# Kernel tuning notes

Hardware: AMD Instinct MI355X
Metric: run time of the kernel (lower is better)

The kernel has to match this reference:

```python
import jax, jax.numpy as jnp
import numpy as np

N = 50000
E = 800000
IN_DIM = 128
HID = 64
HEADS = 4
OUT = 64


def _bn(x, g, b, eps=1e-5):
    # BatchNorm1d with batch statistics (biased var), as in train-mode normalization
    mu = x.mean(0)
    var = ((x - mu) ** 2).mean(0)
    return (x - mu) * jax.lax.rsqrt(var + eps) * g + b


def _gat(x, W, a_src, a_dst, bias, src, dst, heads, dim, concat):
    # PyG GATConv: h = xW; e_ij = LeakyReLU(a_src.h_j + a_dst.h_i); softmax over incoming edges of i
    n = x.shape[0]
    h = (x @ W).reshape(n, heads, dim)            # [N,H,D]
    es = (h * a_src).sum(-1)                      # [N,H]
    ed = (h * a_dst).sum(-1)                      # [N,H]
    e = jax.nn.leaky_relu(es[src] + ed[dst], 0.2)  # [E,H]
    emax = jax.ops.segment_max(e, dst, num_segments=n)
    w = jnp.exp(e - emax[dst])
    denom = jax.ops.segment_sum(w, dst, num_segments=n)
    alpha = w / (denom[dst] + 1e-16)              # [E,H]
    out = jax.ops.segment_sum(h[src] * alpha[:, :, None], dst, num_segments=n)  # [N,H,D]
    out = out.reshape(n, heads * dim) if concat else out.mean(axis=1)
    return out + bias


def _gcn(x, W, bias, src, dst):
    # PyG GCNConv with self-loops (already appended): D^{-1/2} A D^{-1/2} x W
    n = x.shape[0]
    h = x @ W
    deg = jax.ops.segment_sum(jnp.ones(src.shape[0], h.dtype), dst, num_segments=n)
    dinv = jax.lax.rsqrt(jnp.maximum(deg, 1e-12))
    norm = dinv[src] * dinv[dst]                  # [E]
    return jax.ops.segment_sum(h[src] * norm[:, None], dst, num_segments=n) + bias


def setup_inputs() -> dict:
    key = jax.random.key(0)
    ks = jax.random.split(key, 16)
    s = 0.1
    inp = {
        "x": jax.random.normal(ks[0], (N, IN_DIM), jnp.float32),
        "edge_index": jax.random.randint(ks[1], (2, E), 0, N, jnp.int64 if jax.config.jax_enable_x64 else jnp.int32),
        "edge_attr": jax.random.normal(ks[2], (E,), jnp.float32),
        # GAT layer 1
        "W1": jax.random.normal(ks[3], (IN_DIM, HEADS * HID), jnp.float32) * s,
        "att_src1": jax.random.normal(ks[4], (HEADS, HID), jnp.float32) * s,
        "att_dst1": jax.random.normal(ks[5], (HEADS, HID), jnp.float32) * s,
        "b1": jnp.zeros((HEADS * HID,), jnp.float32),
        "g1": jnp.ones((HEADS * HID,), jnp.float32),
        "beta1": jnp.zeros((HEADS * HID,), jnp.float32),
        # GCN
        "Wg": jax.random.normal(ks[6], (HEADS * HID, HID), jnp.float32) * s,
        "bg": jnp.zeros((HID,), jnp.float32),
        "g2": jnp.ones((HID,), jnp.float32),
        "beta2": jnp.zeros((HID,), jnp.float32),
        # GAT layer 2 (heads=1, concat=False)
        "W2": jax.random.normal(ks[7], (HID, OUT), jnp.float32) * s,
        "att_src2": jax.random.normal(ks[8], (1, OUT), jnp.float32) * s,
        "att_dst2": jax.random.normal(ks[9], (1, OUT), jnp.float32) * s,
        "b2": jnp.zeros((OUT,), jnp.float32),
        "g3": jnp.ones((OUT,), jnp.float32),
        "beta3": jnp.zeros((OUT,), jnp.float32),
        # projector
        "Wp1": jax.random.normal(ks[10], (OUT, 128), jnp.float32) * s,
        "bp1": jnp.zeros((128,), jnp.float32),
        "Wp2": jax.random.normal(ks[11], (128, 64), jnp.float32) * s,
        "bp2": jnp.zeros((64,), jnp.float32),
    }
    return inp


def reference(x, edge_index, edge_attr, W1, att_src1, att_dst1, b1, g1, beta1,
              Wg, bg, g2, beta2, W2, att_src2, att_dst2, b2, g3, beta3,
              Wp1, bp1, Wp2, bp2):
    # edge_attr is ignored by GATConv when edge_dim is None (PyG behavior)
    loop = jnp.arange(N, dtype=edge_index.dtype)
    src = jnp.concatenate([edge_index[0], loop])  # self-loops appended
    dst = jnp.concatenate([edge_index[1], loop])
    h = _gat(x, W1, att_src1, att_dst1, b1, src, dst, HEADS, HID, True)
    h = jax.nn.elu(_bn(h, g1, beta1))
    h = _gcn(h, Wg, bg, src, dst)
    h = jax.nn.relu(_bn(h, g2, beta2))
    h = _gat(h, W2, att_src2, att_dst2, b2, src, dst, 1, OUT, False)
    h = jax.nn.elu(_bn(h, g3, beta3))
    return jax.nn.relu(h @ Wp1 + bp1) @ Wp2 + bp2
```

## Files before the change

kernel.cpp:

```cpp
#include <hip/hip_runtime.h>
#include <math.h>

#define NN 50000
#define EE 800000
#define E2 850000
#define SCB 196
#define GXL 391

__device__ __forceinline__ float bf2f(unsigned short u) {
  return __uint_as_float(((unsigned int)u) << 16);
}
__device__ __forceinline__ unsigned short f2bf(float f) {
  unsigned int x = __float_as_uint(f);
  unsigned int r = (x + 0x7fffu + ((x >> 16) & 1u)) >> 16;
  return (unsigned short)r;
}

__device__ __forceinline__ float leaky(float x) { return x > 0.f ? x : 0.2f * x; }

__device__ __forceinline__ int edge_src(const int* ei, int e) {
  return (e < EE) ? ei[e] : (e - EE);
}
__device__ __forceinline__ int edge_dst(const int* ei, int e) {
  return (e < EE) ? ei[EE + e] : (e - EE);
}

__global__ void k_deg(const int* __restrict__ ei, int* __restrict__ deg) {
  int e = blockIdx.x * blockDim.x + threadIdx.x;
  if (e < E2) atomicAdd(&deg[edge_dst(ei, e)], 1);
}

__global__ __launch_bounds__(256) void k_scan1(const int* __restrict__ deg,
                                               int* __restrict__ partial) {
  __shared__ int sd[256];
  int i = blockIdx.x * 256 + threadIdx.x;
  sd[threadIdx.x] = (i < NN) ? deg[i] : 0;
  __syncthreads();
  for (int off = 128; off > 0; off >>= 1) {
    if (threadIdx.x < off) sd[threadIdx.x] += sd[threadIdx.x + off];
    __syncthreads();
  }
  if (threadIdx.x == 0) partial[blockIdx.x] = sd[0];
}

__global__ __launch_bounds__(256) void k_scan3(const int* __restrict__ deg,
                                               const int* __restrict__ partial,
                                               int* __restrict__ rowptr,
                                               int* __restrict__ cnt,
                                               float* __restrict__ dinv) {
  __shared__ int sp[256];
  __shared__ int sd[256];
  int t = threadIdx.x;
  sp[t] = (t < SCB) ? partial[t] : 0;
  __syncthreads();
  for (int off = 1; off < 256; off <<= 1) {
    int v = (t >= off) ? sp[t - off] : 0;
    __syncthreads();
    sp[t] += v;
    __syncthreads();
  }
  int base = (blockIdx.x == 0) ? 0 : sp[blockIdx.x - 1];
  int i = blockIdx.x * 256 + t;
  int v = (i < NN) ? deg[i] : 0;
  sd[t] = v;
  __syncthreads();
  for (int off = 1; off < 256; off <<= 1) {
    int u = (t >= off) ? sd[t - off] : 0;
    __syncthreads();
    sd[t] += u;
    __syncthreads();
  }
  if (i < NN) {
    int excl = base + sd[t] - v;
    rowptr[i] = excl;
    cnt[i] = excl;
    dinv[i] = rsqrtf((float)v);
  }
  if (i == 0) rowptr[NN] = E2;
}

__global__ void k_fill(const int* __restrict__ ei, int* __restrict__ cnt,
                       int* __restrict__ csr) {
  int e = blockIdx.x * blockDim.x + threadIdx.x;
  if (e >= E2) return;
  int d = edge_dst(ei, e);
  int s = edge_src(ei, e);
  int pos = atomicAdd(&cnt[d], 1);
  csr[pos] = s;
}

__global__ __launch_bounds__(256) void k_gemm(
    const float* __restrict__ A, const unsigned short* __restrict__ Abf,
    const float* __restrict__ B, const float* __restrict__ biasOut,
    const float* __restrict__ bnst, const float* __restrict__ bng,
    const float* __restrict__ bnb, int inAct, int outAct,
    float* __restrict__ Cf, unsigned short* __restrict__ Cbf,
    const float* __restrict__ rowScale,
    const float* __restrict__ attSrc, const float* __restrict__ attDst,
    float* __restrict__ esOut, float* __restrict__ edOut, int attMode,
    int M, int K, int NC) {
  __shared__ float As[32][132];
  __shared__ float Bs[32][68];
  __shared__ float sSc[256], sSh[256];
  int t = threadIdx.x;
  int tx = t & 15, ty = t >> 4;
  if (bnst) {
    int c = t;
    if (c < K) {
      float sum = 0.f, sq = 0.f;
      for (int cp = 0; cp < 32; ++cp) {
        sum += bnst[cp * 2 * K + c];
        sq += bnst[cp * 2 * K + K + c];
      }
      const float invN = 1.0f / (float)NN;
      float mu = sum * invN;
      float var = sq * invN - mu * mu;
      float rs = rsqrtf(var + 1e-5f);
      float sc = rs * bng[c];
      sSc[c] = sc;
      sSh[c] = fmaf(-mu, sc, bnb[c]);
    }
    __syncthreads();
  }
  int rowBase = blockIdx.x * 128;
  int colBase = blockIdx.y * 64;
  float acc[8][4];
#pragma unroll
  for (int i = 0; i < 8; ++i)
#pragma unroll
    for (int j = 0; j < 4; ++j) acc[i][j] = 0.f;

  int kq = t & 7;
  int r0 = t >> 3;
  for (int kc = 0; kc < K; kc += 32) {
#pragma unroll
    for (int i2 = 0; i2 < 4; ++i2) {
      int row = r0 + 32 * i2;
      int gr = rowBase + row;
      float4 av = make_float4(0.f, 0.f, 0.f, 0.f);
      if (gr < M) {
        if (Abf) {
          ushort4 u4 = *(const ushort4*)&Abf[(size_t)gr * K + kc + kq * 4];
          av = make_float4(bf2f(u4.x), bf2f(u4.y), bf2f(u4.z), bf2f(u4.w));
        } else {
          av = *(const float4*)&A[(size_t)gr * K + kc + kq * 4];
        }
      }
      if (bnst) {
        int c = kc + kq * 4;
        av.x = fmaf(av.x, sSc[c + 0], sSh[c + 0]);
        av.y = fmaf(av.y, sSc[c + 1], sSh[c + 1]);
        av.z = fmaf(av.z, sSc[c + 2], sSh[c + 2]);
        av.w = fmaf(av.w, sSc[c + 3], sSh[c + 3]);
      }
      if (inAct == 1) {
        av.x = fmaxf(av.x, 0.f); av.y = fmaxf(av.y, 0.f);
        av.z = fmaxf(av.z, 0.f); av.w = fmaxf(av.w, 0.f);
      } else if (inAct == 2) {
        av.x = av.x > 0.f ? av.x : expm1f(av.x);
        av.y = av.y > 0.f ? av.y : expm1f(av.y);
        av.z = av.z > 0.f ? av.z : expm1f(av.z);
        av.w = av.w > 0.f ? av.w : expm1f(av.w);
      }
      As[kq * 4 + 0][row] = av.x;
      As[kq * 4 + 1][row] = av.y;
      As[kq * 4 + 2][row] = av.z;
      As[kq * 4 + 3][row] = av.w;
    }
#pragma unroll
    for (int i2 = 0; i2 < 2; ++i2) {
      int u = t + 256 * i2;
      int c4 = u & 15, kk = u >> 4;
      float4 bv = *(const float4*)&B[(size_t)(kc + kk) * NC + colBase + c4 * 4];
      *(float4*)&Bs[kk][c4 * 4] = bv;
    }
    __syncthreads();
#pragma unroll
    for (int kk = 0; kk < 32; ++kk) {
      float4 a0 = *(const float4*)&As[kk][ty * 8];
      float4 a1 = *(const float4*)&As[kk][ty * 8 + 4];
      float4 bv = *(const float4*)&Bs[kk][tx * 4];
      float a_[8] = {a0.x, a0.y, a0.z, a0.w, a1.x, a1.y, a1.z, a1.w};
      float b_[4] = {bv.x, bv.y, bv.z, bv.w};
#pragma unroll
      for (int i = 0; i < 8; ++i)
#pragma unroll
        for (int j = 0; j < 4; ++j) acc[i][j] = fmaf(a_[i], b_[j], acc[i][j]);
    }
    __syncthreads();
  }

  float4 bb = make_float4(0.f, 0.f, 0.f, 0.f);
  if (biasOut) bb = *(const float4*)&biasOut[colBase + tx * 4];
  float4 as4 = make_float4(0.f, 0.f, 0.f, 0.f), ad4 = as4;
  if (attMode) {
    as4 = *(const float4*)&attSrc[colBase + tx * 4];
    ad4 = *(const float4*)&attDst[colBase + tx * 4];
  }
#pragma unroll
  for (int i = 0; i < 8; ++i) {
    int gr = rowBase + ty * 8 + i;
    if (gr < M) {
      float4 v;
      v.x = acc[i][0] + bb.x;
      v.y = acc[i][1] + bb.y;
      v.z = acc[i][2] + bb.z;
      v.w = acc[i][3] + bb.w;
      if (outAct == 1) {
        v.x = fmaxf(v.x, 0.f); v.y = fmaxf(v.y, 0.f);
        v.z = fmaxf(v.z, 0.f); v.w = fmaxf(v.w, 0.f);
      }
      if (Cf) *(float4*)&Cf[(size_t)gr * NC + colBase + tx * 4] = v;
      if (Cbf) {
        float rs_ = rowScale ? rowScale[gr] : 1.f;
        ushort4 u;
        u.x = f2bf(v.x * rs_); u.y = f2bf(v.y * rs_);
        u.z = f2bf(v.z * rs_); u.w = f2bf(v.w * rs_);
        *(ushort4*)&Cbf[(size_t)gr * NC + colBase + tx * 4] = u;
      }
      if (attMode) {
        float pes = v.x * as4.x + v.y * as4.y + v.z * as4.z + v.w * as4.w;
        float ped = v.x * ad4.x + v.y * ad4.y + v.z * ad4.z + v.w * ad4.w;
#pragma unroll
        for (int off = 8; off > 0; off >>= 1) {
          pes += __shfl_xor(pes, off);
          ped += __shfl_xor(ped, off);
        }
        if (tx == 0) {
          if (attMode == 1) {
            esOut[gr * 4 + blockIdx.y] = pes;
            edOut[gr * 4 + blockIdx.y] = ped;
          } else {
            esOut[gr] = pes;
            edOut[gr] = ped;
          }
        }
      }
    }
  }
}

__global__ __launch_bounds__(256) void k_soft1(const float* __restrict__ es,
                                               const float* __restrict__ ed,
                                               const int* __restrict__ rowptr,
                                               const int* __restrict__ csr,
                                               float* __restrict__ w1) {
  int node = blockIdx.x * 16 + (threadIdx.x >> 4);
  int sub = threadIdx.x & 15;
  int start = rowptr[node], end = rowptr[node + 1];
  float4 edv = *(const float4*)&ed[node * 4];
  float m0 = -1e30f, m1 = -1e30f, m2 = -1e30f, m3 = -1e30f;
  float s0 = 0.f, s1 = 0.f, s2 = 0.f, s3 = 0.f;
  for (int k = start + sub; k < end; k += 16) {
    int s = csr[k];
    float4 esv = *(const float4*)&es[s * 4];
    float e0 = leaky(esv.x + edv.x);
    float e1 = leaky(esv.y + edv.y);
    float e2 = leaky(esv.z + edv.z);
    float e3 = leaky(esv.w + edv.w);
    float mn;
    mn = fmaxf(m0, e0); s0 = s0 * __expf(m0 - mn) + __expf(e0 - mn); m0 = mn;
    mn = fmaxf(m1, e1); s1 = s1 * __expf(m1 - mn) + __expf(e1 - mn); m1 = mn;
    mn = fmaxf(m2, e2); s2 = s2 * __expf(m2 - mn) + __expf(e2 - mn); m2 = mn;
    mn = fmaxf(m3, e3); s3 = s3 * __expf(m3 - mn) + __expf(e3 - mn); m3 = mn;
  }
#pragma unroll
  for (int off = 1; off < 16; off <<= 1) {
    float mo, so, mn;
    mo = __shfl_xor(m0, off); so = __shfl_xor(s0, off);
    mn = fmaxf(m0, mo); s0 = s0 * __expf(m0 - mn) + so * __expf(mo - mn); m0 = mn;
    mo = __shfl_xor(m1, off); so = __shfl_xor(s1, off);
    mn = fmaxf(m1, mo); s1 = s1 * __expf(m1 - mn) + so * __expf(mo - mn); m1 = mn;
    mo = __shfl_xor(m2, off); so = __shfl_xor(s2, off);
    mn = fmaxf(m2, mo); s2 = s2 * __expf(m2 - mn) + so * __expf(mo - mn); m2 = mn;
    mo = __shfl_xor(m3, off); so = __shfl_xor(s3, off);
    mn = fmaxf(m3, mo); s3 = s3 * __expf(m3 - mn) + so * __expf(mo - mn); m3 = mn;
  }
  float i0 = 1.f / (s0 + 1e-16f);
  float i1 = 1.f / (s1 + 1e-16f);
  float i2 = 1.f / (s2 + 1e-16f);
  float i3 = 1.f / (s3 + 1e-16f);
  for (int k = start + sub; k < end; k += 16) {
    int s = csr[k];
    float4 esv = *(const float4*)&es[s * 4];
    w1[k]          = __expf(leaky(esv.x + edv.x) - m0) * i0;
    w1[E2 + k]     = __expf(leaky(esv.y + edv.y) - m1) * i1;
    w1[2 * E2 + k] = __expf(leaky(esv.z + edv.z) - m2) * i2;
    w1[3 * E2 + k] = __expf(leaky(esv.w + edv.w) - m3) * i3;
  }
}

__global__ __launch_bounds__(256) void k_soft2(const float* __restrict__ es,
                                               const float* __restrict__ ed,
                                               const int* __restrict__ rowptr,
                                               const int* __restrict__ csr,
                                               float* __restrict__ w2) {
  int node = blockIdx.x * 16 + (threadIdx.x >> 4);
  int sub = threadIdx.x & 15;
  int start = rowptr[node], end = rowptr[node + 1];
  float edi = ed[node];
  float m = -1e30f, ss = 0.f;
  for (int k = start + sub; k < end; k += 16) {
    float e = leaky(es[csr[k]] + edi);
    float mn = fmaxf(m, e);
    ss = ss * __expf(m - mn) + __expf(e - mn);
    m = mn;
  }
#pragma unroll
  for (int off = 1; off < 16; off <<= 1) {
    float mo = __shfl_xor(m, off);
    float so = __shfl_xor(ss, off);
    float mn = fmaxf(m, mo);
    ss = ss * __expf(m - mn) + so * __expf(mo - mn);
    m = mn;
  }
  float inv = 1.f / (ss + 1e-16f);
  for (int k = start + sub; k < end; k += 16) {
    float e = leaky(es[csr[k]] + edi);
    w2[k] = __expf(e - m) * inv;
  }
}

__global__ __launch_bounds__(256) void k_gat1(const unsigned short* __restrict__ h1b,
                                              const float* __restrict__ w1,
                                              const int* __restrict__ rowptr,
                                              const int* __restrict__ csr,
                                              const float* __restrict__ b1,
                                              unsigned short* __restrict__ outb,
                                              float* __restrict__ st) {
  __shared__ float smS[4][256];
  __shared__ float smQ[4][256];
  int wave = threadIdx.x >> 6;
  int lane = threadIdx.x & 63;
  int i = blockIdx.x * 4 + wave;
  int start = rowptr[i], end = rowptr[i + 1];
  const float* wh = w1 + (size_t)(lane >> 4) * E2;
  float4 acc = make_float4(0.f, 0.f, 0.f, 0.f);
  int k = start;
  for (; k + 4 <= end; k += 4) {
    int sA = csr[k], sB = csr[k + 1], sC = csr[k + 2], sD = csr[k + 3];
    float wA = wh[k], wB = wh[k + 1], wC = wh[k + 2], wD = wh[k + 3];
    ushort4 a0 = *(const ushort4*)&h1b[(size_t)sA * 256 + lane * 4];
    ushort4 a1 = *(const ushort4*)&h1b[(size_t)sB * 256 + lane * 4];
    ushort4 a2 = *(const ushort4*)&h1b[(size_t)sC * 256 + lane * 4];
    ushort4 a3 = *(const ushort4*)&h1b[(size_t)sD * 256 + lane * 4];
    acc.x = fmaf(bf2f(a0.x), wA, fmaf(bf2f(a1.x), wB, fmaf(bf2f(a2.x), wC, fmaf(bf2f(a3.x), wD, acc.x))));
    acc.y = fmaf(bf2f(a0.y), wA, fmaf(bf2f(a1.y), wB, fmaf(bf2f(a2.y), wC, fmaf(bf2f(a3.y), wD, acc.y))));
    acc.z = fmaf(bf2f(a0.z), wA, fmaf(bf2f(a1.z), wB, fmaf(bf2f(a2.z), wC, fmaf(bf2f(a3.z), wD, acc.z))));
    acc.w = fmaf(bf2f(a0.w), wA, fmaf(bf2f(a1.w), wB, fmaf(bf2f(a2.w), wC, fmaf(bf2f(a3.w), wD, acc.w))));
  }
  for (; k < end; ++k) {
    int s = csr[k];
    float wv = wh[k];
    ushort4 a0 = *(const ushort4*)&h1b[(size_t)s * 256 + lane * 4];
    acc.x = fmaf(bf2f(a0.x), wv, acc.x);
    acc.y = fmaf(bf2f(a0.y), wv, acc.y);
    acc.z = fmaf(bf2f(a0.z), wv, acc.z);
    acc.w = fmaf(bf2f(a0.w), wv, acc.w);
  }
  float4 bv = *(const float4*)&b1[lane * 4];
  float4 o;
  o.x = acc.x + bv.x; o.y = acc.y + bv.y; o.z = acc.z + bv.z; o.w = acc.w + bv.w;
  ushort4 u;
  u.x = f2bf(o.x); u.y = f2bf(o.y); u.z = f2bf(o.z); u.w = f2bf(o.w);
  *(ushort4*)&outb[(size_t)i * 256 + lane * 4] = u;
  *(float4*)&smS[wave][lane * 4] = o;
  float4 q = make_float4(o.x * o.x, o.y * o.y, o.z * o.z, o.w * o.w);
  *(float4*)&smQ[wave][lane * 4] = q;
  __syncthreads();
  int c = threadIdx.x;
  float s_ = 0.f, q_ = 0.f;
#pragma unroll
  for (int wv = 0; wv < 4; ++wv) { s_ += smS[wv][c]; q_ += smQ[wv][c]; }
  float* dst = st + (size_t)(blockIdx.x & 31) * 512;
  atomicAdd(&dst[c], s_);
  atomicAdd(&dst[256 + c], q_);
}

__global__ __launch_bounds__(256) void k_gcn(const unsigned short* __restrict__ hgb,
                                             const float* __restrict__ dinv,
                                             const int* __restrict__ rowptr,
                                             const int* __restrict__ csr,
                                             const float* __restrict__ bg,
                                             float* __restrict__ out,
                                             float* __restrict__ st) {
  __shared__ float2 sm[4][64];
  int wave = threadIdx.x >> 6;
  int lane = threadIdx.x & 63;
  int i = blockIdx.x * 4 + wave;
  int start = rowptr[i], end = rowptr[i + 1];
  float acc = 0.f;
  int k = start;
  for (; k + 4 <= end; k += 4) {
    int sA = csr[k], sB = csr[k + 1], sC = csr[k + 2], sD = csr[k + 3];
    acc += bf2f(hgb[(size_t)sA * 64 + lane]) + bf2f(hgb[(size_t)sB * 64 + lane]) +
           bf2f(hgb[(size_t)sC * 64 + lane]) + bf2f(hgb[(size_t)sD * 64 + lane]);
  }
  for (; k < end; ++k) acc += bf2f(hgb[(size_t)csr[k] * 64 + lane]);
  float o = fmaf(acc, dinv[i], bg[lane]);
  out[(size_t)i * 64 + lane] = o;
  sm[wave][lane] = make_float2(o, o * o);
  __syncthreads();
  if (threadIdx.x < 64) {
    int c = threadIdx.x;
    float s_ = 0.f, q_ = 0.f;
#pragma unroll
    for (int wv = 0; wv < 4; ++wv) { float2 v = sm[wv][c]; s_ += v.x; q_ += v.y; }
    float* dst = st + (size_t)(blockIdx.x & 31) * 128;
    atomicAdd(&dst[c], s_);
    atomicAdd(&dst[64 + c], q_);
  }
}

__global__ __launch_bounds__(256) void k_gat2(const unsigned short* __restrict__ h2b,
                                              const float* __restrict__ w2,
                                              const int* __restrict__ rowptr,
                                              const int* __restrict__ csr,
                                              const float* __restrict__ b2,
                                              float* __restrict__ out,
                                              float* __restrict__ st) {
  __shared__ float2 sm[4][64];
  int wave = threadIdx.x >> 6;
  int lane = threadIdx.x & 63;
  int i = blockIdx.x * 4 + wave;
  int start = rowptr[i], end = rowptr[i + 1];
  float acc = 0.f;
  int k = start;
  for (; k + 4 <= end; k += 4) {
    int sA = csr[k], sB = csr[k + 1], sC = csr[k + 2], sD = csr[k + 3];
    float wA = w2[k], wB = w2[k + 1], wC = w2[k + 2], wD = w2[k + 3];
    acc = fmaf(bf2f(h2b[(size_t)sA * 64 + lane]), wA,
          fmaf(bf2f(h2b[(size_t)sB * 64 + lane]), wB,
          fmaf(bf2f(h2b[(size_t)sC * 64 + lane]), wC,
          fmaf(bf2f(h2b[(size_t)sD * 64 + lane]), wD, acc))));
  }
  for (; k < end; ++k)
    acc = fmaf(bf2f(h2b[(size_t)csr[k] * 64 + lane]), w2[k], acc);
  float o = acc + b2[lane];
  out[(size_t)i * 64 + lane] = o;
  sm[wave][lane] = make_float2(o, o * o);
  __syncthreads();
  if (threadIdx.x < 64) {
    int c = threadIdx.x;
    float s_ = 0.f, q_ = 0.f;
#pragma unroll
    for (int wv = 0; wv < 4; ++wv) { float2 v = sm[wv][c]; s_ += v.x; q_ += v.y; }
    float* dst = st + (size_t)(blockIdx.x & 31) * 128;
    atomicAdd(&dst[c], s_);
    atomicAdd(&dst[64 + c], q_);
  }
}

extern "C" void kernel_launch(void* const* d_in, const int* in_sizes, int n_in,
                              void* d_out, int out_size, void* d_ws, size_t ws_size,
                              hipStream_t stream) {
  const float* x        = (const float*)d_in[0];
  const int*   ei       = (const int*)d_in[1];
  const float* W1       = (const float*)d_in[3];
  const float* att_src1 = (const float*)d_in[4];
  const float* att_dst1 = (const float*)d_in[5];
  const float* b1       = (const float*)d_in[6];
  const float* g1       = (const float*)d_in[7];
  const float* beta1    = (const float*)d_in[8];
  const float* Wg       = (const float*)d_in[9];
  const float* bg       = (const float*)d_in[10];
  const float* g2       = (const float*)d_in[11];
  const float* beta2    = (const float*)d_in[12];
  const float* W2       = (const float*)d_in[13];
  const float* att_src2 = (const float*)d_in[14];
  const float* att_dst2 = (const float*)d_in[15];
  const float* b2       = (const float*)d_in[16];
  const float* g3       = (const float*)d_in[17];
  const float* beta3    = (const float*)d_in[18];
  const float* Wp1      = (const float*)d_in[19];
  const float* bp1      = (const float*)d_in[20];
  const float* Wp2      = (const float*)d_in[21];
  const float* bp2      = (const float*)d_in[22];
  float* out = (float*)d_out;

  char* w = (char*)d_ws;
  unsigned short* bufBb  = (unsigned short*)(w + 0);
  float*          bufD   = (float*)(w + 0);
  unsigned short* h1b    = (unsigned short*)(w + 51200000);
  float*          hidden = (float*)(w + 51200000);
  float*          w1     = (float*)(w + 76800000);
  float*          w2     = (float*)(w + 76800000);
  unsigned short* hgb    = (unsigned short*)(w + 90400000);
  float*          bufC   = (float*)(w + 96800000);
  unsigned short* h2b    = (unsigned short*)(w + 109600000);
  float*          es1    = (float*)(w + 116000000);
  float*          ed1    = (float*)(w + 116800000);
  float*          es2    = (float*)(w + 117600000);
  float*          ed2    = (float*)(w + 117800000);
  float*          dinv   = (float*)(w + 118000000);
  int*            deg    = (int*)(w + 118200000);
  int*            rowptr = (int*)(w + 118400000);
  int*            cnt    = (int*)(w + 118600064);
  int*            csr    = (int*)(w + 118800064);
  float*          st1    = (float*)(w + 122200064);
  float*          st2    = st1 + 32 * 512;
  float*          st3    = st2 + 32 * 128;
  int*            partial= (int*)(st3 + 32 * 128);

  hipMemsetAsync(deg, 0, NN * sizeof(int), stream);
  hipMemsetAsync(st1, 0, (32 * 512 + 32 * 128 + 32 * 128) * sizeof(float), stream);

  const int EB = (E2 + 255) / 256;
  const int WB = NN / 4;
  const int SB = NN / 16;

  k_deg<<<EB, 256, 0, stream>>>(ei, deg);
  k_scan1<<<SCB, 256, 0, stream>>>(deg, partial);
  k_scan3<<<SCB, 256, 0, stream>>>(deg, partial, rowptr, cnt, dinv);
  k_fill<<<EB, 256, 0, stream>>>(ei, cnt, csr);

  k_gemm<<<dim3(GXL, 4), 256, 0, stream>>>(x, nullptr, W1, nullptr,
                                           nullptr, nullptr, nullptr, 0, 0,
                                           nullptr, h1b, nullptr,
                                           att_src1, att_dst1, es1, ed1, 1,
                                           NN, 128, 256);
  k_soft1<<<SB, 256, 0, stream>>>(es1, ed1, rowptr, csr, w1);
  k_gat1<<<WB, 256, 0, stream>>>(h1b, w1, rowptr, csr, b1, bufBb, st1);

  k_gemm<<<dim3(GXL, 1), 256, 0, stream>>>(nullptr, bufBb, Wg, nullptr,
                                           st1, g1, beta1, 2, 0,
                                           nullptr, hgb, dinv,
                                           nullptr, nullptr, nullptr, nullptr, 0,
                                           NN, 256, 64);
  k_gcn<<<WB, 256, 0, stream>>>(hgb, dinv, rowptr, csr, bg, bufC, st2);

  k_gemm<<<dim3(GXL, 1), 256, 0, stream>>>(bufC, nullptr, W2, nullptr,
                                           st2, g2, beta2, 1, 0,
                                           nullptr, h2b, nullptr,
                                           att_src2, att_dst2, es2, ed2, 2,
                                           NN, 64, 64);
  k_soft2<<<SB, 256, 0, stream>>>(es2, ed2, rowptr, csr, w2);
  k_gat2<<<WB, 256, 0, stream>>>(h2b, w2, rowptr, csr, b2, bufD, st3);

  k_gemm<<<dim3(GXL, 2), 256, 0, stream>>>(bufD, nullptr, Wp1, bp1,
                                           st3, g3, beta3, 2, 1,
                                           hidden, nullptr, nullptr,
                                           nullptr, nullptr, nullptr, nullptr, 0,
                                           NN, 64, 128);
  k_gemm<<<dim3(GXL, 1), 256, 0, stream>>>(hidden, nullptr, Wp2, bp2,
                                           nullptr, nullptr, nullptr, 0, 0,
                                           out, nullptr, nullptr,
                                           nullptr, nullptr, nullptr, nullptr, 0,
                                           NN, 128, 64);
}
```

Measured before the change: 532.4 us.

## Replace FP32 SIMT GEMM with templated bf16 MFMA GEMM kernel

Rewrites the shared GEMM kernel to use 16x16x32 bf16 MFMA instructions. Each wave computes a 32x64 tile, with A fragments loaded straight from global memory and B converted to bf16 and transposed into LDS. The kernel is templated on K, attention mode, input activation and BN use, so branches resolve at compile time. The aim is to cut GEMM compute time across all five dense layers. The cost is reduced input precision (fp32 x and hidden converted to bf16) and uncoalesced scalar output stores.

```diff
diff --git a/kernel.cpp b/kernel.cpp
--- a/kernel.cpp
+++ b/kernel.cpp
@@ -6,6 +6,9 @@
 #define E2 850000
 #define SCB 196
 #define GXL 391
+
+typedef __attribute__((ext_vector_type(8))) short short8;
+typedef __attribute__((ext_vector_type(4))) float float4v;
 
 __device__ __forceinline__ float bf2f(unsigned short u) {
   return __uint_as_float(((unsigned int)u) << 16);
@@ -89,22 +92,28 @@
   csr[pos] = s;
 }
 
-__global__ __launch_bounds__(256) void k_gemm(
+template <int K, int ATTMODE, int INACT, bool ABF, bool USEBN>
+__global__ __launch_bounds__(256) void k_gemm_mfma(
     const float* __restrict__ A, const unsigned short* __restrict__ Abf,
     const float* __restrict__ B, const float* __restrict__ biasOut,
     const float* __restrict__ bnst, const float* __restrict__ bng,
-    const float* __restrict__ bnb, int inAct, int outAct,
+    const float* __restrict__ bnb, int outAct,
     float* __restrict__ Cf, unsigned short* __restrict__ Cbf,
     const float* __restrict__ rowScale,
     const float* __restrict__ attSrc, const float* __restrict__ attDst,
-    float* __restrict__ esOut, float* __restrict__ edOut, int attMode,
-    int M, int K, int NC) {
-  __shared__ float As[32][132];
-  __shared__ float Bs[32][68];
+    float* __restrict__ esOut, float* __restrict__ edOut,
+    int M, int NC) {
+  __shared__ unsigned short BT[64][K + 8];
   __shared__ float sSc[256], sSh[256];
   int t = threadIdx.x;
-  int tx = t & 15, ty = t >> 4;
-  if (bnst) {
+  int lane = t & 63;
+  int wv = t >> 6;
+  int cl = lane & 15;
+  int kg = lane >> 4;
+  int rowBase = blockIdx.x * 128;
+  int colBase = blockIdx.y * 64;
+
+  if (USEBN) {
     int c = t;
     if (c < K) {
       float sum = 0.f, sq = 0.f;
@@ -120,119 +129,124 @@
       sSc[c] = sc;
       sSh[c] = fmaf(-mu, sc, bnb[c]);
     }
-    __syncthreads();
-  }
-  int rowBase = blockIdx.x * 128;
-  int colBase = blockIdx.y * 64;
-  float acc[8][4];
-#pragma unroll
-  for (int i = 0; i < 8; ++i)
-#pragma unroll
-    for (int j = 0; j < 4; ++j) acc[i][j] = 0.f;
-
-  int kq = t & 7;
-  int r0 = t >> 3;
+  }
+  {
+    int c = t & 63;
+    for (int k = t >> 6; k < K; k += 4)
+      BT[c][k] = f2bf(B[(size_t)k * NC + colBase + c]);
+  }
+  __syncthreads();
+
+  float4v acc[2][4];
+#pragma unroll
+  for (int rt = 0; rt < 2; ++rt)
+#pragma unroll
+    for (int ct = 0; ct < 4; ++ct) acc[rt][ct] = (float4v){0.f, 0.f, 0.f, 0.f};
+
+  int grA0 = rowBase + wv * 32 + cl;
+  int grA1 = grA0 + 16;
+
+#pragma unroll
   for (int kc = 0; kc < K; kc += 32) {
-#pragma unroll
-    for (int i2 = 0; i2 < 4; ++i2) {
-      int row = r0 + 32 * i2;
-      int gr = rowBase + row;
-      float4 av = make_float4(0.f, 0.f, 0.f, 0.f);
+    int k0 = kc + kg * 8;
+    short8 afr[2];
+#pragma unroll
+    for (int rt = 0; rt < 2; ++rt) {
+      int gr = rt ? grA1 : grA0;
+      float v[8];
       if (gr < M) {
-        if (Abf) {
-          ushort4 u4 = *(const ushort4*)&Abf[(size_t)gr * K + kc + kq * 4];
-          av = make_float4(bf2f(u4.x), bf2f(u4.y), bf2f(u4.z), bf2f(u4.w));
+        if (ABF) {
+          ushort4 u0 = *(const ushort4*)&Abf[(size_t)gr * K + k0];
+          ushort4 u1 = *(const ushort4*)&Abf[(size_t)gr * K + k0 + 4];
+          v[0] = bf2f(u0.x); v[1] = bf2f(u0.y); v[2] = bf2f(u0.z); v[3] = bf2f(u0.w);
+          v[4] = bf2f(u1.x); v[5] = bf2f(u1.y); v[6] = bf2f(u1.z); v[7] = bf2f(u1.w);
         } else {
-          av = *(const float4*)&A[(size_t)gr * K + kc + kq * 4];
+          float4 f0 = *(const float4*)&A[(size_t)gr * K + k0];
+          float4 f1 = *(const float4*)&A[(size_t)gr * K + k0 + 4];
+          v[0] = f0.x; v[1] = f0.y; v[2] = f0.z; v[3] = f0.w;
+          v[4] = f1.x; v[5] = f1.y; v[6] = f1.z; v[7] = f1.w;
+        }
+      } else {
+#pragma unroll
+        for (int i = 0; i < 8; ++i) v[i] = 0.f;
+      }
+#pragma unroll
+      for (int i = 0; i < 8; ++i) {
+        float x = v[i];
+        if (USEBN) x = fmaf(x, sSc[k0 + i], sSh[k0 + i]);
+        if (INACT == 1) x = fmaxf(x, 0.f);
+        else if (INACT == 2) x = (x > 0.f) ? x : expm1f(x);
+        afr[rt][i] = (short)f2bf(x);
+      }
+    }
+    short8 bfr[4];
+#pragma unroll
+    for (int ct = 0; ct < 4; ++ct)
+      bfr[ct] = *(const short8*)&BT[ct * 16 + cl][k0];
+#pragma unroll
+    for (int rt = 0; rt < 2; ++rt)
+#pragma unroll
+      for (int ct = 0; ct < 4; ++ct)
+        acc[rt][ct] = __builtin_amdgcn_mfma_f32_16x16x32_bf16(
+            afr[rt], bfr[ct], acc[rt][ct], 0, 0, 0);
+  }
+
+  float bb[4], as4[4], ad4[4];
+#pragma unroll
+  for (int ct = 0; ct < 4; ++ct) {
+    int gc = colBase + ct * 16 + cl;
+    bb[ct] = biasOut ? biasOut[gc] : 0.f;
+    if (ATTMODE) {
+      as4[ct] = attSrc[gc];
+      ad4[ct] = attDst[gc];
+    }
+  }
+#pragma unroll
+  for (int rt = 0; rt < 2; ++rt) {
+    float pes[4] = {0.f, 0.f, 0.f, 0.f};
+    float ped[4] = {0.f, 0.f, 0.f, 0.f};
+#pragma unroll
+    for (int reg = 0; reg < 4; ++reg) {
+      int gr = rowBase + wv * 32 + rt * 16 + kg * 4 + reg;
+      bool ok = gr < M;
+      float rs_ = 1.f;
+      if (ok && Cbf && rowScale) rs_ = rowScale[gr];
+#pragma unroll
+      for (int ct = 0; ct < 4; ++ct) {
+        float v = acc[rt][ct][reg] + bb[ct];
+        if (outAct == 1) v = fmaxf(v, 0.f);
+        int gc = colBase + ct * 16 + cl;
+        if (ok) {
+          if (Cf) Cf[(size_t)gr * NC + gc] = v;
+          if (Cbf) Cbf[(size_t)gr * NC + gc] = f2bf(v * rs_);
+        }
+        if (ATTMODE) {
+          pes[reg] = fmaf(v, as4[ct], pes[reg]);
+          ped[reg] = fmaf(v, ad4[ct], ped[reg]);
         }
       }
-      if (bnst) {
-        int c = kc + kq * 4;
-        av.x = fmaf(av.x, sSc[c + 0], sSh[c + 0]);
-        av.y = fmaf(av.y, sSc[c + 1], sSh[c + 1]);
-        av.z = fmaf(av.z, sSc[c + 2], sSh[c + 2]);
-        av.w = fmaf(av.w, sSc[c + 3], sSh[c + 3]);
+    }
+    if (ATTMODE) {
+#pragma unroll
+      for (int reg = 0; reg < 4; ++reg) {
+#pragma unroll
+        for (int off = 8; off > 0; off >>= 1) {
+          pes[reg] += __shfl_xor(pes[reg], off);
+          ped[reg] += __shfl_xor(ped[reg], off);
+        }
       }
-      if (inAct == 1) {
-        av.x = fmaxf(av.x, 0.f); av.y = fmaxf(av.y, 0.f);
-        av.z = fmaxf(av.z, 0.f); av.w = fmaxf(av.w, 0.f);
-      } else if (inAct == 2) {
-        av.x = av.x > 0.f ? av.x : expm1f(av.x);
-        av.y = av.y > 0.f ? av.y : expm1f(av.y);
-        av.z = av.z > 0.f ? av.z : expm1f(av.z);
-        av.w = av.w > 0.f ? av.w : expm1f(av.w);
-      }
-      As[kq * 4 + 0][row] = av.x;
-      As[kq * 4 + 1][row] = av.y;
-      As[kq * 4 + 2][row] = av.z;
-      As[kq * 4 + 3][row] = av.w;
-    }
-#pragma unroll
-    for (int i2 = 0; i2 < 2; ++i2) {
-      int u = t + 256 * i2;
-      int c4 = u & 15, kk = u >> 4;
-      float4 bv = *(const float4*)&B[(size_t)(kc + kk) * NC + colBase + c4 * 4];
-      *(float4*)&Bs[kk][c4 * 4] = bv;
-    }
-    __syncthreads();
-#pragma unroll
-    for (int kk = 0; kk < 32; ++kk) {
-      float4 a0 = *(const float4*)&As[kk][ty * 8];
-      float4 a1 = *(const float4*)&As[kk][ty * 8 + 4];
-      float4 bv = *(const float4*)&Bs[kk][tx * 4];
-      float a_[8] = {a0.x, a0.y, a0.z, a0.w, a1.x, a1.y, a1.z, a1.w};
-      float b_[4] = {bv.x, bv.y, bv.z, bv.w};
-#pragma unroll
-      for (int i = 0; i < 8; ++i)
-#pragma unroll
-        for (int j = 0; j < 4; ++j) acc[i][j] = fmaf(a_[i], b_[j], acc[i][j]);
-    }
-    __syncthreads();
-  }
-
-  float4 bb = make_float4(0.f, 0.f, 0.f, 0.f);
-  if (biasOut) bb = *(const float4*)&biasOut[colBase + tx * 4];
-  float4 as4 = make_float4(0.f, 0.f, 0.f, 0.f), ad4 = as4;
-  if (attMode) {
-    as4 = *(const float4*)&attSrc[colBase + tx * 4];
-    ad4 = *(const float4*)&attDst[colBase + tx * 4];
-  }
-#pragma unroll
-  for (int i = 0; i < 8; ++i) {
-    int gr = rowBase + ty * 8 + i;
-    if (gr < M) {
-      float4 v;
-      v.x = acc[i][0] + bb.x;
-      v.y = acc[i][1] + bb.y;
-      v.z = acc[i][2] + bb.z;
-      v.w = acc[i][3] + bb.w;
-      if (outAct == 1) {
-        v.x = fmaxf(v.x, 0.f); v.y = fmaxf(v.y, 0.f);
-        v.z = fmaxf(v.z, 0.f); v.w = fmaxf(v.w, 0.f);
-      }
-      if (Cf) *(float4*)&Cf[(size_t)gr * NC + colBase + tx * 4] = v;
-      if (Cbf) {
-        float rs_ = rowScale ? rowScale[gr] : 1.f;
-        ushort4 u;
-        u.x = f2bf(v.x * rs_); u.y = f2bf(v.y * rs_);
-        u.z = f2bf(v.z * rs_); u.w = f2bf(v.w * rs_);
-        *(ushort4*)&Cbf[(size_t)gr * NC + colBase + tx * 4] = u;
-      }
-      if (attMode) {
-        float pes = v.x * as4.x + v.y * as4.y + v.z * as4.z + v.w * as4.w;
-        float ped = v.x * ad4.x + v.y * ad4.y + v.z * ad4.z + v.w * ad4.w;
-#pragma unroll
-        for (int off = 8; off > 0; off >>= 1) {
-          pes += __shfl_xor(pes, off);
-          ped += __shfl_xor(ped, off);
-        }
-        if (tx == 0) {
-          if (attMode == 1) {
-            esOut[gr * 4 + blockIdx.y] = pes;
-            edOut[gr * 4 + blockIdx.y] = ped;
-          } else {
-            esOut[gr] = pes;
-            edOut[gr] = ped;
+      if (cl == 0) {
+#pragma unroll
+        for (int reg = 0; reg < 4; ++reg) {
+          int gr = rowBase + wv * 32 + rt * 16 + kg * 4 + reg;
+          if (gr < M) {
+            if (ATTMODE == 1) {
+              esOut[gr * 4 + blockIdx.y] = pes[reg];
+              edOut[gr * 4 + blockIdx.y] = ped[reg];
+            } else {
+              esOut[gr] = pes[reg];
+              edOut[gr] = ped[reg];
+            }
           }
         }
       }
@@ -514,37 +528,27 @@
   k_scan3<<<SCB, 256, 0, stream>>>(deg, partial, rowptr, cnt, dinv);
   k_fill<<<EB, 256, 0, stream>>>(ei, cnt, csr);
 
-  k_gemm<<<dim3(GXL, 4), 256, 0, stream>>>(x, nullptr, W1, nullptr,
-                                           nullptr, nullptr, nullptr, 0, 0,
-                                           nullptr, h1b, nullptr,
-                                           att_src1, att_dst1, es1, ed1, 1,
-                                           NN, 128, 256);
+  k_gemm_mfma<128, 1, 0, false, false><<<dim3(GXL, 4), 256, 0, stream>>>(
+      x, nullptr, W1, nullptr, nullptr, nullptr, nullptr, 0,
+      nullptr, h1b, nullptr, att_src1, att_dst1, es1, ed1, NN, 256);
   k_soft1<<<SB, 256, 0, stream>>>(es1, ed1, rowptr, csr, w1);
   k_gat1<<<WB, 256, 0, stream>>>(h1b, w1, rowptr, csr, b1, bufBb, st1);
 
-  k_gemm<<<dim3(GXL, 1), 256, 0, stream>>>(nullptr, bufBb, Wg, nullptr,
-                                           st1, g1, beta1, 2, 0,
-                                           nullptr, hgb, dinv,
-                                           nullptr, nullptr, nullptr, nullptr, 0,
-                                           NN, 256, 64);
+  k_gemm_mfma<256, 0, 2, true, true><<<dim3(GXL, 1), 256, 0, stream>>>(
+      nullptr, bufBb, Wg, nullptr, st1, g1, beta1, 0,
+      nullptr, hgb, dinv, nullptr, nullptr, nullptr, nullptr, NN, 64);
   k_gcn<<<WB, 256, 0, stream>>>(hgb, dinv, rowptr, csr, bg, bufC, st2);
 
-  k_gemm<<<dim3(GXL, 1), 256, 0, stream>>>(bufC, nullptr, W2, nullptr,
-                                           st2, g2, beta2, 1, 0,
-                                           nullptr, h2b, nullptr,
-                                           att_src2, att_dst2, es2, ed2, 2,
-                                           NN, 64, 64);
+  k_gemm_mfma<64, 2, 1, false, true><<<dim3(GXL, 1), 256, 0, stream>>>(
+      bufC, nullptr, W2, nullptr, st2, g2, beta2, 0,
+      nullptr, h2b, nullptr, att_src2, att_dst2, es2, ed2, NN, 64);
   k_soft2<<<SB, 256, 0, stream>>>(es2, ed2, rowptr, csr, w2);
   k_gat2<<<WB, 256, 0, stream>>>(h2b, w2, rowptr, csr, b2, bufD, st3);
 
-  k_gemm<<<dim3(GXL, 2), 256, 0, stream>>>(bufD, nullptr, Wp1, bp1,
-                                           st3, g3, beta3, 2, 1,
-                                           hidden, nullptr, nullptr,
-                                           nullptr, nullptr, nullptr, nullptr, 0,
-                                           NN, 64, 128);
-  k_gemm<<<dim3(GXL, 1), 256, 0, stream>>>(hidden, nullptr, Wp2, bp2,
-                                           nullptr, nullptr, nullptr, 0, 0,
-                                           out, nullptr, nullptr,
-                                           nullptr, nullptr, nullptr, nullptr, 0,
-                                           NN, 128, 64);
-}
+  k_gemm_mfma<64, 0, 2, false, true><<<dim3(GXL, 2), 256, 0, stream>>>(
+      bufD, nullptr, Wp1, bp1, st3, g3, beta3, 1,
+      hidden, nullptr, nullptr, nullptr, nullptr, nullptr, nullptr, NN, 128);
+  k_gemm_mfma<128, 0, 0, false, false><<<dim3(GXL, 1), 256, 0, stream>>>(
+      hidden, nullptr, Wp2, bp2, nullptr, nullptr, nullptr, 0,
+      out, nullptr, nullptr, nullptr, nullptr, nullptr, nullptr, NN, 64);
+}
```

Measured after the change: 485.4 us. 1.1x faster.
